# Optimization experiments

Hardware: AMD Instinct MI355X
Metric: run time of the kernel (lower is better)

## Reference

```python
import jax, jax.numpy as jnp
import numpy as np

IN_F, OUT_F, GRID = 1024, 1024, 8
B = 8192
GRID_LO, GRID_HI = -1.0, 1.0


def setup_inputs() -> dict:
    key = jax.random.key(0)
    k1, k2 = jax.random.split(key)
    x = jax.random.normal(k1, (B, IN_F), dtype=jnp.float32)
    # buffers: grid is linspace expanded over in_features; sigma = 1.5*h
    h = (GRID_HI - GRID_LO) / (GRID - 1)
    grid = jnp.broadcast_to(jnp.linspace(GRID_LO, GRID_HI, GRID, dtype=jnp.float32), (IN_F, GRID))
    sigma = jnp.float32(1.5 * h)
    # params
    scale_base = jnp.ones((IN_F, OUT_F), dtype=jnp.float32)
    scale_spline = jnp.ones((IN_F, OUT_F), dtype=jnp.float32)
    # kaiming_uniform-ish init: bound = sqrt(6/fan_in)/sqrt(1+a^2) approximated by small uniform
    fan_in = IN_F * GRID
    gain = np.sqrt(2.0 / (1.0 + 5.0 * 0.1 * 0.1))
    bound = gain * np.sqrt(3.0 / fan_in)
    spline_weight = jax.random.uniform(k2, (OUT_F, IN_F, GRID), dtype=jnp.float32, minval=-bound, maxval=bound)
    return {"x": x, "scale_base": scale_base, "spline_weight": spline_weight,
            "scale_spline": scale_spline, "grid": grid, "sigma": sigma}


def reference(x, scale_base, spline_weight, scale_spline, grid, sigma):
    # x: [B, I]; grid: [I, G]; spline_weight: [O, I, G]; scales: [I, O]
    base_out = jnp.einsum('bi,io->bo', jax.nn.silu(x), scale_base)
    # RBF bases: exp(-((x - grid)/sigma)^2)  -> [B, I, G]
    bases = jnp.exp(-jnp.square((x[:, :, None] - grid[None, :, :]) / sigma))
    # fused spline contraction (mathematically identical to big,oig->bio then bio,io->bo)
    spline_out = jnp.einsum('big,oig,io->bo', bases, spline_weight, scale_spline)
    return base_out + spline_out
```

## Files before the change

### kernel.cpp

```cpp
#include <hip/hip_runtime.h>


#define BATCH 8192
#define IN_F  1024
#define OUT_F 1024
#define GRID_N 8
#define K2    (IN_F * GRID_N)
#define KTOT  (IN_F + K2)

#define BM 128
#define BN 128
#define BK 64
#define BK8 128

typedef __bf16 bf16x8 __attribute__((ext_vector_type(8)));
typedef float  f32x4  __attribute__((ext_vector_type(4)));
typedef int    int32x8 __attribute__((ext_vector_type(8)));

__device__ __forceinline__ void gl2lds16(const void* g, void* l) {
  __builtin_amdgcn_global_load_lds(
      (const __attribute__((address_space(1))) void*)g,
      (__attribute__((address_space(3))) void*)l, 16, 0, 0);
}

__device__ __forceinline__ void pack_fp8x8(const float* v, int& w0, int& w1) {
  w0 = 0; w1 = 0;
  w0 = __builtin_amdgcn_cvt_pk_fp8_f32(v[0], v[1], w0, false);
  w0 = __builtin_amdgcn_cvt_pk_fp8_f32(v[2], v[3], w0, true);
  w1 = __builtin_amdgcn_cvt_pk_fp8_f32(v[4], v[5], w1, false);
  w1 = __builtin_amdgcn_cvt_pk_fp8_f32(v[6], v[7], w1, true);
}

__global__ __launch_bounds__(256)
void kan_mix(const float* __restrict__ x, const float* __restrict__ sb,
             const float* __restrict__ sw, const float* __restrict__ ss,
             const float* __restrict__ grid, const float* __restrict__ sigma,
             __bf16* __restrict__ sbT, unsigned char* __restrict__ wbt8,
             unsigned char* __restrict__ Ab8, __bf16* __restrict__ sbA) {
  const int t = threadIdx.x;
  const int bx = blockIdx.x;
  if (bx < 256) {
    __shared__ float tile[64][65];
    const int o0 = (bx & 15) * 64, k0 = (bx >> 4) * 64;
    const int r = t >> 4, c4 = (t & 15) * 4;
    #pragma unroll
    for (int it = 0; it < 4; ++it) {
      const int k = k0 + r + it * 16;
      float4 v = *(const float4*)(sb + (size_t)k * OUT_F + o0 + c4);
      tile[r + it * 16][c4 + 0] = v.x; tile[r + it * 16][c4 + 1] = v.y;
      tile[r + it * 16][c4 + 2] = v.z; tile[r + it * 16][c4 + 3] = v.w;
    }
    __syncthreads();
    #pragma unroll
    for (int it = 0; it < 4; ++it) {
      const int ol = r + it * 16;
      union { __bf16 h[4]; uint2 q; } s;
      #pragma unroll
      for (int e = 0; e < 4; ++e) s.h[e] = (__bf16)tile[c4 + e][ol];
      *(uint2*)(sbT + (size_t)(o0 + ol) * IN_F + k0 + c4) = s.q;
    }
  } else if (bx < 512) {
    __shared__ float tile[64][65];
    const int sp = bx - 256;
    const int o0 = (sp >> 4) * 64;
    const int j0 = (sp & 15) * 512;
    const int i0 = j0 >> 3;
    const int r = t >> 4, c4 = (t & 15) * 4;
    #pragma unroll
    for (int it = 0; it < 4; ++it) {
      const int i = i0 + r + it * 16;
      float4 v = *(const float4*)(ss + (size_t)i * OUT_F + o0 + c4);
      tile[r + it * 16][c4 + 0] = v.x; tile[r + it * 16][c4 + 1] = v.y;
      tile[r + it * 16][c4 + 2] = v.z; tile[r + it * 16][c4 + 3] = v.w;
    }
    __syncthreads();
    #pragma unroll
    for (int p = 0; p < 16; ++p) {
      const int f = p * 256 + t;
      const int o_l = f >> 6, i_l = f & 63;
      const float sc = tile[i_l][o_l];
      const float* swp = sw + (size_t)(o0 + o_l) * K2 + j0 + i_l * 8;
      float4 a = *(const float4*)swp;
      float4 b = *(const float4*)(swp + 4);
      float vv[8] = {a.x * sc, a.y * sc, a.z * sc, a.w * sc,
                     b.x * sc, b.y * sc, b.z * sc, b.w * sc};
      int w0, w1; pack_fp8x8(vv, w0, w1);
      *(int2*)(wbt8 + (size_t)(o0 + o_l) * K2 + j0 + i_l * 8) = make_int2(w0, w1);
    }
  } else {
    const int b = bx - 512;
    const float inv_sigma = 1.0f / sigma[0];
    const float* xrow = x + (size_t)b * IN_F;
    unsigned char* arow = Ab8 + (size_t)b * K2;
    __bf16* srow = sbA + (size_t)b * IN_F;
    {
      float4 v = ((const float4*)xrow)[t];
      float vv[4] = {v.x, v.y, v.z, v.w};
      union { __bf16 h[4]; uint2 q; } s;
      #pragma unroll
      for (int e = 0; e < 4; ++e) s.h[e] = (__bf16)(vv[e] / (1.0f + __expf(-vv[e])));
      ((uint2*)srow)[t] = s.q;
    }
    #pragma unroll
    for (int it = 0; it < 4; ++it) {
      const int i = t + it * 256;
      const float u = xrow[i];
      float4 g0 = *(const float4*)(grid + (size_t)i * GRID_N);
      float4 g1 = *(const float4*)(grid + (size_t)i * GRID_N + 4);
      float gg[8] = {g0.x, g0.y, g0.z, g0.w, g1.x, g1.y, g1.z, g1.w};
      float bb[8];
      #pragma unroll
      for (int g = 0; g < GRID_N; ++g) {
        float d = (u - gg[g]) * inv_sigma;
        bb[g] = __expf(-d * d);
      }
      int w0, w1; pack_fp8x8(bb, w0, w1);
      *(int2*)(arow + (size_t)i * GRID_N) = make_int2(w0, w1);
    }
  }
}

__global__ __launch_bounds__(256)
void kan_gemm_all(const unsigned char* __restrict__ Ab8,
                  const unsigned char* __restrict__ wbt8,
                  const __bf16* __restrict__ sbA,
                  const __bf16* __restrict__ sbT,
                  float* __restrict__ out) {
  __shared__ unsigned char smem[2][32768];

  const int tid = threadIdx.x;
  const int bx  = blockIdx.x;
  const int s   = bx >> 3;
  const int r0  = ((bx & 7) * 8 + (s >> 3)) * BM;
  const int c0  = (s & 7) * BN;

  const int lane = tid & 63, wave = tid >> 6;
  const int wm = wave & 1, wn = wave >> 1;
  const int quad = lane >> 4, l15 = lane & 15;

  int a_off8[4][2], b_off8[4][2];
  #pragma unroll
  for (int t4 = 0; t4 < 4; ++t4) {
    const int rowA = wm * 64 + t4 * 16 + l15;
    const int rowB = wn * 64 + t4 * 16 + l15;
    #pragma unroll
    for (int h = 0; h < 2; ++h) {
      a_off8[t4][h] = rowA * BK8 + (((quad * 2 + h) ^ (rowA & 7)) * 16);
      b_off8[t4][h] = 16384 + rowB * BK8 + (((quad * 2 + h) ^ (rowB & 7)) * 16);
    }
  }
  int a_off16[2][4], b_off16[2][4];
  #pragma unroll
  for (int ks = 0; ks < 2; ++ks) {
    const int kc = ks * 4 + quad;
    #pragma unroll
    for (int t4 = 0; t4 < 4; ++t4) {
      const int rowA = wm * 64 + t4 * 16 + l15;
      a_off16[ks][t4] = (rowA * 8 + (kc ^ (rowA & 7))) * 16;
      const int rowB = wn * 64 + t4 * 16 + l15;
      b_off16[ks][t4] = 16384 + (rowB * 8 + (kc ^ (rowB & 7))) * 16;
    }
  }

  const unsigned char* aSrc8[4]; const unsigned char* bSrc8[4];
  const __bf16* aSrc16[4]; const __bf16* bSrc16[4]; int dstOff[4];
  #pragma unroll
  for (int it = 0; it < 4; ++it) {
    const int p = it * 256 + tid;
    const int row = p >> 3;
    const int kc  = (p & 7) ^ (row & 7);
    aSrc8[it]  = Ab8  + (size_t)(r0 + row) * K2 + kc * 16;
    bSrc8[it]  = wbt8 + (size_t)(c0 + row) * K2 + kc * 16;
    aSrc16[it] = sbA  + (size_t)(r0 + row) * IN_F + kc * 8;
    bSrc16[it] = sbT  + (size_t)(c0 + row) * IN_F + kc * 8;
    dstOff[it] = p * 16;
  }

  f32x4 zero; zero[0] = 0.f; zero[1] = 0.f; zero[2] = 0.f; zero[3] = 0.f;
  f32x4 acc[4][4];
  #pragma unroll
  for (int a = 0; a < 4; ++a)
    #pragma unroll
    for (int b = 0; b < 4; ++b) acc[a][b] = zero;

  #pragma unroll
  for (int it = 0; it < 4; ++it) {
    gl2lds16(aSrc8[it], &smem[0][dstOff[it]]);
    gl2lds16(bSrc8[it], &smem[0][16384 + dstOff[it]]);
  }
  asm volatile("s_waitcnt vmcnt(0)" ::: "memory");
  __builtin_amdgcn_s_barrier();
  asm volatile("" ::: "memory");

  int cur = 0;
  for (int t = 0; t < 64; ++t) {
    const int nxt = cur ^ 1;
    if (t < 63) {
      const int kb = (t + 1) * BK8;
      #pragma unroll
      for (int it = 0; it < 4; ++it) {
        gl2lds16(aSrc8[it] + kb, &smem[nxt][dstOff[it]]);
        gl2lds16(bSrc8[it] + kb, &smem[nxt][16384 + dstOff[it]]);
      }
    } else {
      #pragma unroll
      for (int it = 0; it < 4; ++it) {
        gl2lds16(aSrc16[it], &smem[nxt][dstOff[it]]);
        gl2lds16(bSrc16[it], &smem[nxt][16384 + dstOff[it]]);
      }
    }
    const unsigned char* sp = smem[cur];
    union frag { int32x8 v; uint4 q[2]; };
    frag af[4], bfv[4];
    #pragma unroll
    for (int t4 = 0; t4 < 4; ++t4) {
      af[t4].q[0]  = *(const uint4*)(sp + a_off8[t4][0]);
      af[t4].q[1]  = *(const uint4*)(sp + a_off8[t4][1]);
      bfv[t4].q[0] = *(const uint4*)(sp + b_off8[t4][0]);
      bfv[t4].q[1] = *(const uint4*)(sp + b_off8[t4][1]);
    }
    __builtin_amdgcn_s_setprio(1);
    #pragma unroll
    for (int tm = 0; tm < 4; ++tm)
      #pragma unroll
      for (int tn = 0; tn < 4; ++tn)
        acc[tm][tn] = __builtin_amdgcn_mfma_scale_f32_16x16x128_f8f6f4(
            af[tm].v, bfv[tn].v, acc[tm][tn],
            0, 0, 0, 0x7F7F7F7F, 0, 0x7F7F7F7F);
    __builtin_amdgcn_s_setprio(0);
    asm volatile("s_waitcnt vmcnt(0)" ::: "memory");
    __builtin_amdgcn_sched_barrier(0);
    __builtin_amdgcn_s_barrier();
    asm volatile("" ::: "memory");
    cur = nxt;
  }

  for (int t = 0; t < 16; ++t) {
    const int nxt = cur ^ 1;
    if (t < 15) {
      const int ke = (t + 1) * BK;
      #pragma unroll
      for (int it = 0; it < 4; ++it) {
        gl2lds16(aSrc16[it] + ke, &smem[nxt][dstOff[it]]);
        gl2lds16(bSrc16[it] + ke, &smem[nxt][16384 + dstOff[it]]);
      }
    }
    const unsigned char* sp = smem[cur];
    #pragma unroll
    for (int ks = 0; ks < 2; ++ks) {
      bf16x8 af[4], bfv[4];
      #pragma unroll
      for (int t4 = 0; t4 < 4; ++t4) af[t4]  = *(const bf16x8*)(sp + a_off16[ks][t4]);
      #pragma unroll
      for (int t4 = 0; t4 < 4; ++t4) bfv[t4] = *(const bf16x8*)(sp + b_off16[ks][t4]);
      __builtin_amdgcn_s_setprio(1);
      #pragma unroll
      for (int tm = 0; tm < 4; ++tm)
        #pragma unroll
        for (int tn = 0; tn < 4; ++tn)
          acc[tm][tn] = __builtin_amdgcn_mfma_f32_16x16x32_bf16(
              af[tm], bfv[tn], acc[tm][tn], 0, 0, 0);
      __builtin_amdgcn_s_setprio(0);
    }
    asm volatile("s_waitcnt vmcnt(0)" ::: "memory");
    __builtin_amdgcn_sched_barrier(0);
    __builtin_amdgcn_s_barrier();
    asm volatile("" ::: "memory");
    cur = nxt;
  }

  #pragma unroll
  for (int tm = 0; tm < 4; ++tm) {
    const int row = r0 + wm * 64 + tm * 16 + quad * 4;
    #pragma unroll
    for (int tn = 0; tn < 4; ++tn) {
      const int col = c0 + wn * 64 + tn * 16 + l15;
      float* op = out + (size_t)row * OUT_F + col;
      #pragma unroll
      for (int r = 0; r < 4; ++r)
        op[(size_t)r * OUT_F] = acc[tm][tn][r];
    }
  }
}

__global__ __launch_bounds__(256)
void kan_prep_w_full(const float* __restrict__ sb, const float* __restrict__ sw,
                     const float* __restrict__ ss, __bf16* __restrict__ wbt) {
  const int t = threadIdx.x;
  if (blockIdx.x < 256) {
    __shared__ float tile[64][65];
    const int o0 = (blockIdx.x & 15) * 64, k0 = (blockIdx.x >> 4) * 64;
    const int r = t >> 4, c4 = (t & 15) * 4;
    #pragma unroll
    for (int it = 0; it < 4; ++it) {
      const int k = k0 + r + it * 16;
      float4 v = *(const float4*)(sb + (size_t)k * OUT_F + o0 + c4);
      tile[r + it * 16][c4 + 0] = v.x; tile[r + it * 16][c4 + 1] = v.y;
      tile[r + it * 16][c4 + 2] = v.z; tile[r + it * 16][c4 + 3] = v.w;
    }
    __syncthreads();
    #pragma unroll
    for (int it = 0; it < 4; ++it) {
      const int ol = r + it * 16;
      union { __bf16 h[4]; uint2 q; } s;
      #pragma unroll
      for (int e = 0; e < 4; ++e) s.h[e] = (__bf16)tile[c4 + e][ol];
      *(uint2*)(wbt + (size_t)(o0 + ol) * KTOT + k0 + c4) = s.q;
    }
  } else {
    const size_t e = ((size_t)(blockIdx.x - 256) * 256 + t) * 8;
    const int o = (int)(e >> 13);
    const int j = (int)(e & 8191);
    const int i = j >> 3;
    const float sc = ss[(size_t)i * OUT_F + o];
    float4 a = *(const float4*)(sw + e);
    float4 b = *(const float4*)(sw + e + 4);
    float vv[8] = {a.x, a.y, a.z, a.w, b.x, b.y, b.z, b.w};
    union { __bf16 h[8]; uint4 q; } s;
    #pragma unroll
    for (int g = 0; g < 8; ++g) s.h[g] = (__bf16)(vv[g] * sc);
    *(uint4*)(wbt + (size_t)o * KTOT + IN_F + j) = s.q;
  }
}

__global__ __launch_bounds__(256, 2)
void kan_gemm_fused(const float* __restrict__ x, const __bf16* __restrict__ wbt,
                    const float* __restrict__ grid, const float* __restrict__ sigma,
                    float* __restrict__ out) {
  __shared__ __bf16 As[BM * BK];
  __shared__ __bf16 Bs[BN * BK];
  __shared__ float  gLds[IN_F * GRID_N];
  const int tid = threadIdx.x;
  const int bx  = blockIdx.x;
  const int c0  = (bx & 7) * BN;
  const int r0  = (bx >> 3) * BM;
  for (int idx = tid; idx < IN_F * GRID_N / 4; idx += 256)
    ((float4*)gLds)[idx] = ((const float4*)grid)[idx];
  const float inv_sigma = 1.0f / sigma[0];
  const int lane = tid & 63, wave = tid >> 6;
  const int wm = wave & 1, wn = wave >> 1;
  const int quad = lane >> 4, l15 = lane & 15;
  f32x4 zero; zero[0] = 0.f; zero[1] = 0.f; zero[2] = 0.f; zero[3] = 0.f;
  f32x4 acc[4][4];
  #pragma unroll
  for (int a = 0; a < 4; ++a)
    #pragma unroll
    for (int b = 0; b < 4; ++b) acc[a][b] = zero;
  const int m = tid >> 1, half = tid & 1;
  const float* xrow = x + (size_t)(r0 + m) * IN_F;
  __syncthreads();
  for (int kb = 0; kb < KTOT; kb += BK) {
    union { __bf16 h[32]; uint4 q[4]; } av;
    if (kb < IN_F) {
      const float4* xp = (const float4*)(xrow + kb + half * 32);
      #pragma unroll
      for (int j4 = 0; j4 < 8; ++j4) {
        float4 v = xp[j4];
        float vv[4] = {v.x, v.y, v.z, v.w};
        #pragma unroll
        for (int e = 0; e < 4; ++e)
          av.h[j4 * 4 + e] = (__bf16)(vv[e] / (1.0f + __expf(-vv[e])));
      }
    } else {
      const int i0 = (kb - IN_F) >> 3;
      float4 xv = *(const float4*)(xrow + i0 + half * 4);
      float xs[4] = {xv.x, xv.y, xv.z, xv.w};
      #pragma unroll
      for (int ii = 0; ii < 4; ++ii) {
        const float u = xs[ii];
        const float* gp = &gLds[(i0 + half * 4 + ii) * GRID_N];
        #pragma unroll
        for (int g = 0; g < GRID_N; ++g) {
          float d = (u - gp[g]) * inv_sigma;
          av.h[ii * 8 + g] = (__bf16)__expf(-d * d);
        }
      }
    }
    __syncthreads();
    {
      uint4* dst = (uint4*)&As[m * BK + half * 32];
      #pragma unroll
      for (int qd = 0; qd < 4; ++qd) dst[qd] = av.q[qd];
    }
    #pragma unroll
    for (int it = 0; it < 4; ++it) {
      const int idx = it * 2048 + tid * 8;
      const int n = idx >> 6, k = idx & 63;
      gl2lds16(wbt + (size_t)(c0 + n) * KTOT + kb + k, &Bs[idx]);
    }
    __syncthreads();
    #pragma unroll
    for (int ks = 0; ks < 2; ++ks) {
      bf16x8 af[4], bfv[4];
      #pragma unroll
      for (int t4 = 0; t4 < 4; ++t4)
        af[t4] = *(const bf16x8*)&As[(wm * 64 + t4 * 16 + l15) * BK + ks * 32 + quad * 8];
      #pragma unroll
      for (int t4 = 0; t4 < 4; ++t4)
        bfv[t4] = *(const bf16x8*)&Bs[(wn * 64 + t4 * 16 + l15) * BK + ks * 32 + quad * 8];
      #pragma unroll
      for (int tm = 0; tm < 4; ++tm)
        #pragma unroll
        for (int tn = 0; tn < 4; ++tn)
          acc[tm][tn] = __builtin_amdgcn_mfma_f32_16x16x32_bf16(
              af[tm], bfv[tn], acc[tm][tn], 0, 0, 0);
    }
  }
  #pragma unroll
  for (int tm = 0; tm < 4; ++tm) {
    const int row = r0 + wm * 64 + tm * 16 + quad * 4;
    #pragma unroll
    for (int tn = 0; tn < 4; ++tn) {
      const int col = c0 + wn * 64 + tn * 16 + l15;
      float* op = out + (size_t)row * OUT_F + col;
      #pragma unroll
      for (int r = 0; r < 4; ++r)
        op[(size_t)r * OUT_F] = acc[tm][tn][r];
    }
  }
}

extern "C" void kernel_launch(void* const* d_in, const int* in_sizes, int n_in,
                              void* d_out, int out_size, void* d_ws, size_t ws_size,
                              hipStream_t stream) {
  const float* x     = (const float*)d_in[0];
  const float* sb    = (const float*)d_in[1];
  const float* sw    = (const float*)d_in[2];
  const float* ss    = (const float*)d_in[3];
  const float* grid  = (const float*)d_in[4];
  const float* sigma = (const float*)d_in[5];
  float* out = (float*)d_out;

  const size_t SBT_BYTES = (size_t)OUT_F * IN_F * 2;
  const size_t WS_BYTES  = (size_t)OUT_F * K2;
  const size_t A_BYTES   = (size_t)BATCH * K2;
  const size_t SBA_BYTES = (size_t)BATCH * IN_F * 2;

  if (ws_size >= SBT_BYTES + WS_BYTES + A_BYTES + SBA_BYTES) {
    __bf16*        sbT  = (__bf16*)d_ws;
    unsigned char* wbt8 = (unsigned char*)d_ws + SBT_BYTES;
    unsigned char* Ab8  = (unsigned char*)d_ws + SBT_BYTES + WS_BYTES;
    __bf16*        sbA  = (__bf16*)((char*)d_ws + SBT_BYTES + WS_BYTES + A_BYTES);
    kan_mix<<<dim3(512 + BATCH), dim3(256), 0, stream>>>(
        x, sb, sw, ss, grid, sigma, sbT, wbt8, Ab8, sbA);
    kan_gemm_all<<<dim3((BATCH / BM) * (OUT_F / BN)), dim3(256), 0, stream>>>(
        Ab8, wbt8, sbA, sbT, out);
  } else {
    __bf16* wbt = (__bf16*)d_ws;
    kan_prep_w_full<<<dim3(4352), dim3(256), 0, stream>>>(sb, sw, ss, wbt);
    kan_gemm_fused<<<dim3((BATCH / BM) * (OUT_F / BN)), dim3(256), 0, stream>>>(
        x, wbt, grid, sigma, out);
  }
}
```

Baseline: 227.8 us.

## Load B fragments directly from global into registers, halving LDS per block

The GEMM kernel stops staging the weight (B) tile through shared memory. Each wave now loads its B fragments straight from global memory into registers, double-buffered across an unrolled two-stage loop, while the A tile stays on the global-to-LDS path. This halves LDS use to 32 KB and adds a launch-bounds hint of two blocks per CU, aiming for more occupancy and less LDS traffic. In exchange, each wave reads B from global/L2 redundantly (the two wm waves load the same B rows) and register pressure rises from the extra fragment buffers.

```diff
diff --git a/kernel.cpp b/kernel.cpp
--- a/kernel.cpp
+++ b/kernel.cpp
@@ -16,6 +16,8 @@
 typedef __bf16 bf16x8 __attribute__((ext_vector_type(8)));
 typedef float  f32x4  __attribute__((ext_vector_type(4)));
 typedef int    int32x8 __attribute__((ext_vector_type(8)));
+
+union frag { int32x8 v; uint4 q[2]; };
 
 __device__ __forceinline__ void gl2lds16(const void* g, void* l) {
   __builtin_amdgcn_global_load_lds(
@@ -120,13 +122,13 @@
   }
 }
 
-__global__ __launch_bounds__(256)
+__global__ __launch_bounds__(256, 2)
 void kan_gemm_all(const unsigned char* __restrict__ Ab8,
                   const unsigned char* __restrict__ wbt8,
                   const __bf16* __restrict__ sbA,
                   const __bf16* __restrict__ sbT,
                   float* __restrict__ out) {
-  __shared__ unsigned char smem[2][32768];
+  __shared__ unsigned char smem[2][16384];
 
   const int tid = threadIdx.x;
   const int bx  = blockIdx.x;
@@ -138,18 +140,15 @@
   const int wm = wave & 1, wn = wave >> 1;
   const int quad = lane >> 4, l15 = lane & 15;
 
-  int a_off8[4][2], b_off8[4][2];
+  int a_off8[4][2];
   #pragma unroll
   for (int t4 = 0; t4 < 4; ++t4) {
     const int rowA = wm * 64 + t4 * 16 + l15;
-    const int rowB = wn * 64 + t4 * 16 + l15;
-    #pragma unroll
-    for (int h = 0; h < 2; ++h) {
+    #pragma unroll
+    for (int h = 0; h < 2; ++h)
       a_off8[t4][h] = rowA * BK8 + (((quad * 2 + h) ^ (rowA & 7)) * 16);
-      b_off8[t4][h] = 16384 + rowB * BK8 + (((quad * 2 + h) ^ (rowB & 7)) * 16);
-    }
-  }
-  int a_off16[2][4], b_off16[2][4];
+  }
+  int a_off16[2][4];
   #pragma unroll
   for (int ks = 0; ks < 2; ++ks) {
     const int kc = ks * 4 + quad;
@@ -157,23 +156,26 @@
     for (int t4 = 0; t4 < 4; ++t4) {
       const int rowA = wm * 64 + t4 * 16 + l15;
       a_off16[ks][t4] = (rowA * 8 + (kc ^ (rowA & 7))) * 16;
-      const int rowB = wn * 64 + t4 * 16 + l15;
-      b_off16[ks][t4] = 16384 + (rowB * 8 + (kc ^ (rowB & 7))) * 16;
-    }
-  }
-
-  const unsigned char* aSrc8[4]; const unsigned char* bSrc8[4];
-  const __bf16* aSrc16[4]; const __bf16* bSrc16[4]; int dstOff[4];
+    }
+  }
+
+  const unsigned char* aSrc8[4]; const __bf16* aSrc16[4]; int dstOff[4];
   #pragma unroll
   for (int it = 0; it < 4; ++it) {
     const int p = it * 256 + tid;
     const int row = p >> 3;
     const int kc  = (p & 7) ^ (row & 7);
-    aSrc8[it]  = Ab8  + (size_t)(r0 + row) * K2 + kc * 16;
-    bSrc8[it]  = wbt8 + (size_t)(c0 + row) * K2 + kc * 16;
-    aSrc16[it] = sbA  + (size_t)(r0 + row) * IN_F + kc * 8;
-    bSrc16[it] = sbT  + (size_t)(c0 + row) * IN_F + kc * 8;
+    aSrc8[it]  = Ab8 + (size_t)(r0 + row) * K2 + kc * 16;
+    aSrc16[it] = sbA + (size_t)(r0 + row) * IN_F + kc * 8;
     dstOff[it] = p * 16;
+  }
+
+  const unsigned char* bDir8[4]; const __bf16* bDir16[4];
+  #pragma unroll
+  for (int t4 = 0; t4 < 4; ++t4) {
+    const int rowB = wn * 64 + t4 * 16 + l15;
+    bDir8[t4]  = wbt8 + (size_t)(c0 + rowB) * K2 + quad * 32;
+    bDir16[t4] = sbT + (size_t)(c0 + rowB) * IN_F + quad * 8;
   }
 
   f32x4 zero; zero[0] = 0.f; zero[1] = 0.f; zero[2] = 0.f; zero[3] = 0.f;
@@ -183,90 +185,111 @@
     #pragma unroll
     for (int b = 0; b < 4; ++b) acc[a][b] = zero;
 
-  #pragma unroll
-  for (int it = 0; it < 4; ++it) {
-    gl2lds16(aSrc8[it], &smem[0][dstOff[it]]);
-    gl2lds16(bSrc8[it], &smem[0][16384 + dstOff[it]]);
-  }
-  asm volatile("s_waitcnt vmcnt(0)" ::: "memory");
-  __builtin_amdgcn_s_barrier();
-  asm volatile("" ::: "memory");
-
-  int cur = 0;
-  for (int t = 0; t < 64; ++t) {
-    const int nxt = cur ^ 1;
-    if (t < 63) {
-      const int kb = (t + 1) * BK8;
-      #pragma unroll
-      for (int it = 0; it < 4; ++it) {
-        gl2lds16(aSrc8[it] + kb, &smem[nxt][dstOff[it]]);
-        gl2lds16(bSrc8[it] + kb, &smem[nxt][16384 + dstOff[it]]);
-      }
-    } else {
-      #pragma unroll
-      for (int it = 0; it < 4; ++it) {
-        gl2lds16(aSrc16[it], &smem[nxt][dstOff[it]]);
-        gl2lds16(bSrc16[it], &smem[nxt][16384 + dstOff[it]]);
-      }
-    }
-    const unsigned char* sp = smem[cur];
-    union frag { int32x8 v; uint4 q[2]; };
-    frag af[4], bfv[4];
+  frag bA[4], bB[4];
+  bf16x8 b16A[2][4], b16B[2][4];
+
+  auto loadB8 = [&](frag (&bv)[4], int kb) {
     #pragma unroll
     for (int t4 = 0; t4 < 4; ++t4) {
-      af[t4].q[0]  = *(const uint4*)(sp + a_off8[t4][0]);
-      af[t4].q[1]  = *(const uint4*)(sp + a_off8[t4][1]);
-      bfv[t4].q[0] = *(const uint4*)(sp + b_off8[t4][0]);
-      bfv[t4].q[1] = *(const uint4*)(sp + b_off8[t4][1]);
-    }
-    __builtin_amdgcn_s_setprio(1);
-    #pragma unroll
-    for (int tm = 0; tm < 4; ++tm)
-      #pragma unroll
-      for (int tn = 0; tn < 4; ++tn)
-        acc[tm][tn] = __builtin_amdgcn_mfma_scale_f32_16x16x128_f8f6f4(
-            af[tm].v, bfv[tn].v, acc[tm][tn],
-            0, 0, 0, 0x7F7F7F7F, 0, 0x7F7F7F7F);
-    __builtin_amdgcn_s_setprio(0);
+      bv[t4].q[0] = *(const uint4*)(bDir8[t4] + kb);
+      bv[t4].q[1] = *(const uint4*)(bDir8[t4] + kb + 16);
+    }
+  };
+  auto loadB16 = [&](bf16x8 (&bv)[2][4], int ke) {
+    #pragma unroll
+    for (int t4 = 0; t4 < 4; ++t4)
+      #pragma unroll
+      for (int ks = 0; ks < 2; ++ks)
+        bv[ks][t4] = *(const bf16x8*)(bDir16[t4] + ke + ks * 32);
+  };
+  auto stageA8 = [&](unsigned char* buf, int kb) {
+    #pragma unroll
+    for (int it = 0; it < 4; ++it) gl2lds16(aSrc8[it] + kb, buf + dstOff[it]);
+  };
+  auto stageA16 = [&](unsigned char* buf, int ke) {
+    #pragma unroll
+    for (int it = 0; it < 4; ++it) gl2lds16(aSrc16[it] + ke, buf + dstOff[it]);
+  };
+  auto endbar = [&]() {
     asm volatile("s_waitcnt vmcnt(0)" ::: "memory");
     __builtin_amdgcn_sched_barrier(0);
     __builtin_amdgcn_s_barrier();
     asm volatile("" ::: "memory");
-    cur = nxt;
-  }
-
-  for (int t = 0; t < 16; ++t) {
-    const int nxt = cur ^ 1;
-    if (t < 15) {
-      const int ke = (t + 1) * BK;
-      #pragma unroll
-      for (int it = 0; it < 4; ++it) {
-        gl2lds16(aSrc16[it] + ke, &smem[nxt][dstOff[it]]);
-        gl2lds16(bSrc16[it] + ke, &smem[nxt][16384 + dstOff[it]]);
-      }
-    }
-    const unsigned char* sp = smem[cur];
-    #pragma unroll
-    for (int ks = 0; ks < 2; ++ks) {
-      bf16x8 af[4], bfv[4];
-      #pragma unroll
-      for (int t4 = 0; t4 < 4; ++t4) af[t4]  = *(const bf16x8*)(sp + a_off16[ks][t4]);
-      #pragma unroll
-      for (int t4 = 0; t4 < 4; ++t4) bfv[t4] = *(const bf16x8*)(sp + b_off16[ks][t4]);
+  };
+  auto fp8_compute = [&](const unsigned char* sp, frag (&bv)[4]) {
+    #pragma unroll
+    for (int tm = 0; tm < 4; ++tm) {
+      frag af;
+      af.q[0] = *(const uint4*)(sp + a_off8[tm][0]);
+      af.q[1] = *(const uint4*)(sp + a_off8[tm][1]);
       __builtin_amdgcn_s_setprio(1);
       #pragma unroll
-      for (int tm = 0; tm < 4; ++tm)
+      for (int tn = 0; tn < 4; ++tn)
+        acc[tm][tn] = __builtin_amdgcn_mfma_scale_f32_16x16x128_f8f6f4(
+            af.v, bv[tn].v, acc[tm][tn], 0, 0, 0, 0x7F7F7F7F, 0, 0x7F7F7F7F);
+      __builtin_amdgcn_s_setprio(0);
+    }
+  };
+  auto bf16_compute = [&](const unsigned char* sp, bf16x8 (&bv)[2][4]) {
+    #pragma unroll
+    for (int ks = 0; ks < 2; ++ks)
+      #pragma unroll
+      for (int tm = 0; tm < 4; ++tm) {
+        bf16x8 af = *(const bf16x8*)(sp + a_off16[ks][tm]);
+        __builtin_amdgcn_s_setprio(1);
         #pragma unroll
         for (int tn = 0; tn < 4; ++tn)
           acc[tm][tn] = __builtin_amdgcn_mfma_f32_16x16x32_bf16(
-              af[tm], bfv[tn], acc[tm][tn], 0, 0, 0);
-      __builtin_amdgcn_s_setprio(0);
-    }
-    asm volatile("s_waitcnt vmcnt(0)" ::: "memory");
-    __builtin_amdgcn_sched_barrier(0);
-    __builtin_amdgcn_s_barrier();
-    asm volatile("" ::: "memory");
-    cur = nxt;
+              af, bv[ks][tn], acc[tm][tn], 0, 0, 0);
+        __builtin_amdgcn_s_setprio(0);
+      }
+  };
+
+  loadB8(bA, 0);
+  stageA8(&smem[0][0], 0);
+  asm volatile("s_waitcnt vmcnt(0)" ::: "memory");
+  __builtin_amdgcn_s_barrier();
+  asm volatile("" ::: "memory");
+
+  for (int tt = 0; tt < 32; ++tt) {
+    {
+      const int kb = (2 * tt + 1) * BK8;
+      loadB8(bB, kb);
+      stageA8(&smem[1][0], kb);
+      fp8_compute(&smem[0][0], bA);
+      endbar();
+    }
+    {
+      if (tt < 31) {
+        const int kb = (2 * tt + 2) * BK8;
+        loadB8(bA, kb);
+        stageA8(&smem[0][0], kb);
+      } else {
+        loadB16(b16A, 0);
+        stageA16(&smem[0][0], 0);
+      }
+      fp8_compute(&smem[1][0], bB);
+      endbar();
+    }
+  }
+
+  for (int ss = 0; ss < 8; ++ss) {
+    {
+      const int ke = (2 * ss + 1) * BK;
+      loadB16(b16B, ke);
+      stageA16(&smem[1][0], ke);
+      bf16_compute(&smem[0][0], b16A);
+      endbar();
+    }
+    {
+      if (ss < 7) {
+        const int ke = (2 * ss + 2) * BK;
+        loadB16(b16A, ke);
+        stageA16(&smem[0][0], ke);
+      }
+      bf16_compute(&smem[1][0], b16B);
+      if (ss < 7) endbar();
+    }
   }
 
   #pragma unroll
```

Measured after the change: 312.7 us. 1.37x slower.
